# Optimization experiments

Hardware: AMD Instinct MI355X
Metric: run time of the kernel (lower is better)

Reference implementation:

```python
import jax, jax.numpy as jnp
import numpy as np

B, N, M, CIN, C, COUT = 4, 2048, 8192, 1, 2, 64  # C = in_channels + density channel
EPS = 1e-8


def setup_inputs() -> dict:
    key = jax.random.key(0)
    k0, k1, k2, k3 = jax.random.split(key, 4)
    context_in = jax.random.normal(k0, (B, N, 1), dtype=jnp.float32)
    context_out = jax.random.normal(k1, (B, N, CIN), dtype=jnp.float32)
    target_in = jax.random.normal(k2, (B, M, 1), dtype=jnp.float32)
    sigma = jnp.zeros((C,), dtype=jnp.float32)  # log(init_length_scale=1.0) = 0
    # Xavier-normal init for projection Linear(C -> COUT): std = sqrt(2/(C+COUT))
    W = jax.random.normal(k3, (COUT, C), dtype=jnp.float32) * np.sqrt(2.0 / (C + COUT)).astype(np.float32)
    b = jnp.zeros((COUT,), dtype=jnp.float32)
    return {"context_in": context_in, "context_out": context_out,
            "target_in": target_in, "sigma": sigma, "W": W, "b": b}


def reference(context_in, context_out, target_in, sigma, W, b):
    # Pairwise squared distances: (B, N, M)
    dists = jnp.sum((context_in[:, :, None, :] - target_in[:, None, :, :]) ** 2, axis=-1)
    # Per-channel RBF weights: (B, N, M, C)
    scales = jnp.exp(sigma)  # (C,)
    weights = jnp.exp(-0.5 * dists[..., None] / (scales ** 2))
    # Append density channel (ones) to context outputs: (B, N, C)
    density_ones = jnp.ones(context_out.shape[:2] + (1,), dtype=context_out.dtype)
    ctx = jnp.concatenate([density_ones, context_out], axis=-1)
    # Weighted aggregation over context points: (B, M, C)
    out = jnp.einsum('bnmc,bnc->bmc', weights, ctx)
    # Density normalization of non-density channels
    density, conv = out[..., :1], out[..., 1:]
    conv = conv / (density + EPS)
    out = jnp.concatenate([density, conv], axis=-1)
    # Final linear projection: (B, M, COUT)
    return out @ W.T + b
```

## Files before the change

### kernel.cpp

```cpp
#include <hip/hip_runtime.h>

#define NB    4
#define NN    2048
#define NM    8192
#define NCOUT 64

__device__ __forceinline__ float fexp2(float x) {
#if defined(__has_builtin)
#if __has_builtin(__builtin_amdgcn_exp2f)
    return __builtin_amdgcn_exp2f(x);
#else
    return exp2f(x);
#endif
#else
    return exp2f(x);
#endif
}

__global__ __launch_bounds__(256) void convcnp_kernel(
    const float* __restrict__ ci,
    const float* __restrict__ co,
    const float* __restrict__ ti,
    const float* __restrict__ sigma,
    const float* __restrict__ W,
    const float* __restrict__ bias,
    float* __restrict__ out)
{
    __shared__ float2 sxy[NN];
    const int tid   = threadIdx.x;
    const int bidx  = blockIdx.x;
    const int b     = bidx >> 10;
    const int mbase = (bidx & 1023) * 8;

    const float4* ci4 = (const float4*)(ci + (size_t)b * NN);
    const float4* co4 = (const float4*)(co + (size_t)b * NN);
    #pragma unroll
    for (int i = tid; i < NN / 4; i += 256) {
        float4 x = ci4[i];
        float4 y = co4[i];
        sxy[4 * i + 0] = make_float2(x.x, y.x);
        sxy[4 * i + 1] = make_float2(x.y, y.y);
        sxy[4 * i + 2] = make_float2(x.z, y.z);
        sxy[4 * i + 3] = make_float2(x.w, y.w);
    }

    const float LOG2E = 1.4426950408889634f;
    const float c0 = -0.5f * __expf(-2.0f * sigma[0]) * LOG2E;
    const float c1 = -0.5f * __expf(-2.0f * sigma[1]) * LOG2E;
    __syncthreads();

    const int wave = tid >> 6;
    const int lane = tid & 63;
    const int m0 = mbase + wave * 2;
    const int m1 = m0 + 1;
    const float t0 = ti[(size_t)b * NM + m0];
    const float t1 = ti[(size_t)b * NM + m1];

    float a00 = 0.f, a01 = 0.f;
    float a10 = 0.f, a11 = 0.f;

    if (c0 == c1) {
        #pragma unroll 4
        for (int n = lane; n < NN; n += 64) {
            float2 xy = sxy[n];
            float d0 = xy.x - t0; d0 *= d0;
            float d1 = xy.x - t1; d1 *= d1;
            float w0 = fexp2(c0 * d0);
            float w1 = fexp2(c0 * d1);
            a00 += w0; a01 = fmaf(w0, xy.y, a01);
            a10 += w1; a11 = fmaf(w1, xy.y, a11);
        }
    } else {
        #pragma unroll 2
        for (int n = lane; n < NN; n += 64) {
            float2 xy = sxy[n];
            float d0 = xy.x - t0; d0 *= d0;
            float d1 = xy.x - t1; d1 *= d1;
            float w0a = fexp2(c0 * d0), w0b = fexp2(c1 * d0);
            float w1a = fexp2(c0 * d1), w1b = fexp2(c1 * d1);
            a00 += w0a; a01 = fmaf(w0b, xy.y, a01);
            a10 += w1a; a11 = fmaf(w1b, xy.y, a11);
        }
    }

    #pragma unroll
    for (int off = 32; off > 0; off >>= 1) {
        a00 += __shfl_xor(a00, off, 64);
        a01 += __shfl_xor(a01, off, 64);
        a10 += __shfl_xor(a10, off, 64);
        a11 += __shfl_xor(a11, off, 64);
    }

    const float EPSF = 1e-8f;
    float o0a = a00, o1a = a01 / (a00 + EPSF);
    float o0b = a10, o1b = a11 / (a10 + EPSF);

    float w0 = W[2 * lane], w1 = W[2 * lane + 1], bb = bias[lane];
    out[((size_t)b * NM + m0) * NCOUT + lane] = fmaf(o0a, w0, fmaf(o1a, w1, bb));
    out[((size_t)b * NM + m1) * NCOUT + lane] = fmaf(o0b, w0, fmaf(o1b, w1, bb));
}

extern "C" void kernel_launch(void* const* d_in, const int* in_sizes, int n_in,
                              void* d_out, int out_size, void* d_ws, size_t ws_size,
                              hipStream_t stream) {
    const float* ci    = (const float*)d_in[0];
    const float* co    = (const float*)d_in[1];
    const float* ti    = (const float*)d_in[2];
    const float* sigma = (const float*)d_in[3];
    const float* W     = (const float*)d_in[4];
    const float* bias  = (const float*)d_in[5];
    float* out = (float*)d_out;

    dim3 grid(NB * NM / 8);
    dim3 block(256);
    hipLaunchKernelGGL(convcnp_kernel, grid, block, 0, stream,
                       ci, co, ti, sigma, W, bias, out);
}
```

Measured before the change: 80.24 us.

## Process four targets per wave with packed FMA and sqrt-scaled exponent form

Each wave now handles four target points instead of two, which halves the grid and amortizes the shared-memory staging of context points over twice as many targets. The exponent is rewritten as -(r*x - r*t)^2 using a precomputed sqrt of the scale, so a single FMA plus a multiply produces the argument, and the math is expressed with 2-wide float vectors to encourage packed FP32 instructions. The trade-off is more accumulator registers and fewer blocks, with slightly different rounding in the exponent argument.

```diff
diff --git a/kernel.cpp b/kernel.cpp
--- a/kernel.cpp
+++ b/kernel.cpp
@@ -4,6 +4,8 @@
 #define NN    2048
 #define NM    8192
 #define NCOUT 64
+
+typedef float v2f __attribute__((ext_vector_type(2)));
 
 __device__ __forceinline__ float fexp2(float x) {
 #if defined(__has_builtin)
@@ -28,9 +30,8 @@
 {
     __shared__ float2 sxy[NN];
     const int tid   = threadIdx.x;
-    const int bidx  = blockIdx.x;
-    const int b     = bidx >> 10;
-    const int mbase = (bidx & 1023) * 8;
+    const int b     = blockIdx.x >> 9;
+    const int mbase = (blockIdx.x & 511) * 16;
 
     const float4* ci4 = (const float4*)(ci + (size_t)b * NN);
     const float4* co4 = (const float4*)(co + (size_t)b * NN);
@@ -45,59 +46,87 @@
     }
 
     const float LOG2E = 1.4426950408889634f;
-    const float c0 = -0.5f * __expf(-2.0f * sigma[0]) * LOG2E;
-    const float c1 = -0.5f * __expf(-2.0f * sigma[1]) * LOG2E;
+    const float s0 = sigma[0], s1 = sigma[1];
+    const float k0 = 0.5f * LOG2E * __expf(-2.0f * s0);
+    const float k1 = 0.5f * LOG2E * __expf(-2.0f * s1);
+    const float r0 = sqrtf(k0);
+    const float r1 = sqrtf(k1);
     __syncthreads();
 
     const int wave = tid >> 6;
     const int lane = tid & 63;
-    const int m0 = mbase + wave * 2;
-    const int m1 = m0 + 1;
-    const float t0 = ti[(size_t)b * NM + m0];
-    const float t1 = ti[(size_t)b * NM + m1];
+    const int m0   = mbase + wave * 4;
+    const float* tb = ti + (size_t)b * NM + m0;
+    const float t0 = tb[0], t1 = tb[1], t2 = tb[2], t3 = tb[3];
 
-    float a00 = 0.f, a01 = 0.f;
-    float a10 = 0.f, a11 = 0.f;
+    v2f den01 = {0.f, 0.f}, den23 = {0.f, 0.f};
+    v2f cv01  = {0.f, 0.f}, cv23  = {0.f, 0.f};
 
-    if (c0 == c1) {
+    if (s0 == s1) {
+        const v2f r2    = {r0, r0};
+        const v2f nrt01 = {-r0 * t0, -r0 * t1};
+        const v2f nrt23 = {-r0 * t2, -r0 * t3};
         #pragma unroll 4
         for (int n = lane; n < NN; n += 64) {
             float2 xy = sxy[n];
-            float d0 = xy.x - t0; d0 *= d0;
-            float d1 = xy.x - t1; d1 *= d1;
-            float w0 = fexp2(c0 * d0);
-            float w1 = fexp2(c0 * d1);
-            a00 += w0; a01 = fmaf(w0, xy.y, a01);
-            a10 += w1; a11 = fmaf(w1, xy.y, a11);
+            v2f x2 = {xy.x, xy.x};
+            v2f y2 = {xy.y, xy.y};
+            v2f e01 = x2 * r2 + nrt01;
+            v2f e23 = x2 * r2 + nrt23;
+            v2f f01 = e01 * e01;
+            v2f f23 = e23 * e23;
+            v2f w01, w23;
+            w01.x = fexp2(-f01.x);
+            w01.y = fexp2(-f01.y);
+            w23.x = fexp2(-f23.x);
+            w23.y = fexp2(-f23.y);
+            den01 += w01;
+            den23 += w23;
+            cv01 = w01 * y2 + cv01;
+            cv23 = w23 * y2 + cv23;
         }
     } else {
+        const float a0 = -r0 * t0, a1 = -r0 * t1, a2 = -r0 * t2, a3 = -r0 * t3;
+        const float b0 = -r1 * t0, b1 = -r1 * t1, b2 = -r1 * t2, b3 = -r1 * t3;
         #pragma unroll 2
         for (int n = lane; n < NN; n += 64) {
             float2 xy = sxy[n];
-            float d0 = xy.x - t0; d0 *= d0;
-            float d1 = xy.x - t1; d1 *= d1;
-            float w0a = fexp2(c0 * d0), w0b = fexp2(c1 * d0);
-            float w1a = fexp2(c0 * d1), w1b = fexp2(c1 * d1);
-            a00 += w0a; a01 = fmaf(w0b, xy.y, a01);
-            a10 += w1a; a11 = fmaf(w1b, xy.y, a11);
+            const float x = xy.x, y = xy.y;
+            float ea0 = fmaf(r0, x, a0), ea1 = fmaf(r0, x, a1);
+            float ea2 = fmaf(r0, x, a2), ea3 = fmaf(r0, x, a3);
+            float eb0 = fmaf(r1, x, b0), eb1 = fmaf(r1, x, b1);
+            float eb2 = fmaf(r1, x, b2), eb3 = fmaf(r1, x, b3);
+            den01.x += fexp2(-ea0 * ea0); den01.y += fexp2(-ea1 * ea1);
+            den23.x += fexp2(-ea2 * ea2); den23.y += fexp2(-ea3 * ea3);
+            cv01.x = fmaf(fexp2(-eb0 * eb0), y, cv01.x);
+            cv01.y = fmaf(fexp2(-eb1 * eb1), y, cv01.y);
+            cv23.x = fmaf(fexp2(-eb2 * eb2), y, cv23.x);
+            cv23.y = fmaf(fexp2(-eb3 * eb3), y, cv23.y);
         }
     }
 
     #pragma unroll
     for (int off = 32; off > 0; off >>= 1) {
-        a00 += __shfl_xor(a00, off, 64);
-        a01 += __shfl_xor(a01, off, 64);
-        a10 += __shfl_xor(a10, off, 64);
-        a11 += __shfl_xor(a11, off, 64);
+        den01.x += __shfl_xor(den01.x, off, 64);
+        den01.y += __shfl_xor(den01.y, off, 64);
+        den23.x += __shfl_xor(den23.x, off, 64);
+        den23.y += __shfl_xor(den23.y, off, 64);
+        cv01.x  += __shfl_xor(cv01.x,  off, 64);
+        cv01.y  += __shfl_xor(cv01.y,  off, 64);
+        cv23.x  += __shfl_xor(cv23.x,  off, 64);
+        cv23.y  += __shfl_xor(cv23.y,  off, 64);
     }
 
     const float EPSF = 1e-8f;
-    float o0a = a00, o1a = a01 / (a00 + EPSF);
-    float o0b = a10, o1b = a11 / (a10 + EPSF);
-
-    float w0 = W[2 * lane], w1 = W[2 * lane + 1], bb = bias[lane];
-    out[((size_t)b * NM + m0) * NCOUT + lane] = fmaf(o0a, w0, fmaf(o1a, w1, bb));
-    out[((size_t)b * NM + m1) * NCOUT + lane] = fmaf(o0b, w0, fmaf(o1b, w1, bb));
+    const float den[4] = {den01.x, den01.y, den23.x, den23.y};
+    const float cv[4]  = {cv01.x,  cv01.y,  cv23.x,  cv23.y};
+    const float w0 = W[2 * lane], w1 = W[2 * lane + 1], bb = bias[lane];
+    float* ob = out + ((size_t)b * NM + m0) * NCOUT + lane;
+    #pragma unroll
+    for (int k = 0; k < 4; ++k) {
+        const float conv = cv[k] / (den[k] + EPSF);
+        ob[(size_t)k * NCOUT] = fmaf(den[k], w0, fmaf(conv, w1, bb));
+    }
 }
 
 extern "C" void kernel_launch(void* const* d_in, const int* in_sizes, int n_in,
@@ -111,7 +140,7 @@
     const float* bias  = (const float*)d_in[5];
     float* out = (float*)d_out;
 
-    dim3 grid(NB * NM / 8);
+    dim3 grid(NB * NM / 16);
     dim3 block(256);
     hipLaunchKernelGGL(convcnp_kernel, grid, block, 0, stream,
                        ci, co, ti, sigma, W, bias, out);
```

After: 78.26 us. -2.5%, faster.
